# Performance work log

Hardware: AMD Instinct MI355X
Metric: run time of the kernel (lower is better)

## Reference

```python
import jax, jax.numpy as jnp
import numpy as np

N_NODES = 50000
N_EDGES = 800000
IN_DIM = 128
OUT_DIM = 64
NUM_HEADS = 4


def setup_inputs() -> dict:
    key = jax.random.key(0)
    k1, k2, k3, k4 = jax.random.split(key, 4)
    h = jax.random.normal(k1, (N_NODES, IN_DIM), dtype=jnp.float32)
    # Xavier-uniform-like init for each head's weight
    limit = float(np.sqrt(6.0 / (IN_DIM + OUT_DIM)))
    W = jax.random.uniform(k2, (NUM_HEADS, IN_DIM, OUT_DIM), dtype=jnp.float32, minval=-limit, maxval=limit)
    b = jnp.zeros((OUT_DIM,), dtype=jnp.float32)
    src = jax.random.randint(k3, (N_EDGES,), 0, N_NODES, dtype=jnp.int32)
    dst = jax.random.randint(k4, (N_EDGES,), 0, N_NODES, dtype=jnp.int32)
    return {"h": h, "W": W, "b": b, "src": src, "dst": dst}


def reference(h, W, b, src, dst):
    # Multi-head projection averaged over heads: (1/K) * sum_k h @ W_k  -> [N, out_dim]
    hp = jnp.einsum('nd,kdf->nf', h, W) / W.shape[0]
    # copy_src + sum aggregation: scatter-sum messages h[src] into dst nodes
    msgs = hp[src]  # [E, out_dim]
    agg = jax.ops.segment_sum(msgs, dst, num_segments=h.shape[0])  # [N, out_dim]
    return jax.nn.relu(agg + b)
```

## Files before the change

### kernel.cpp

```cpp
#include <hip/hip_runtime.h>

#define N_NODES 50000
#define N_EDGES 800000
#define IN_DIM 128
#define OUT_DIM 64
#define PAD 64

typedef __attribute__((ext_vector_type(8))) short bf16x8;
typedef __attribute__((ext_vector_type(4))) float f32x4;

__device__ inline unsigned short f2bf(float x) {
    unsigned u = __builtin_bit_cast(unsigned, x);
    unsigned r = (u + 0x7FFFu + ((u >> 16) & 1u)) >> 16;
    return (unsigned short)r;
}

__global__ __launch_bounds__(256) void wavgT_kernel(const float* __restrict__ W,
                                                    unsigned short* __restrict__ wT) {
    __shared__ unsigned short lds[64 * 129];
    const int t = threadIdx.x;
    for (int i = t; i < 8192; i += 256) {
        const int d = i >> 6, f = i & 63;
        float s = W[d * 64 + f] + W[8192 + d * 64 + f] +
                  W[16384 + d * 64 + f] + W[24576 + d * 64 + f];
        lds[f * 129 + d] = f2bf(0.25f * s);
    }
    __syncthreads();
    for (int i = t; i < 8192; i += 256) {
        const int f = i >> 7, d = i & 127;
        wT[i] = lds[f * 129 + d];
    }
}

__global__ __launch_bounds__(256) void gemm_mfma_kernel(const float* __restrict__ h,
                                                        const unsigned short* __restrict__ wT,
                                                        unsigned short* __restrict__ hp) {
    const int wave = (blockIdx.x << 2) + (threadIdx.x >> 6);
    const int n0 = wave << 4;
    if (n0 >= N_NODES) return;
    const int lane = threadIdx.x & 63;
    const int lm = lane & 15;
    const int lg = lane >> 4;

    bf16x8 bfrag[4][4];
#pragma unroll
    for (int nt = 0; nt < 4; ++nt)
#pragma unroll
        for (int ks = 0; ks < 4; ++ks)
            bfrag[nt][ks] = *(const bf16x8*)&wT[(nt * 16 + lm) * 128 + ks * 32 + lg * 8];

    f32x4 acc[4];
#pragma unroll
    for (int nt = 0; nt < 4; ++nt) acc[nt] = (f32x4)0.0f;

    const float* hrow = h + (size_t)(n0 + lm) * IN_DIM;
#pragma unroll
    for (int ks = 0; ks < 4; ++ks) {
        const float4 a0 = *(const float4*)&hrow[ks * 32 + lg * 8];
        const float4 a1 = *(const float4*)&hrow[ks * 32 + lg * 8 + 4];
        bf16x8 af;
        af[0] = (short)f2bf(a0.x); af[1] = (short)f2bf(a0.y);
        af[2] = (short)f2bf(a0.z); af[3] = (short)f2bf(a0.w);
        af[4] = (short)f2bf(a1.x); af[5] = (short)f2bf(a1.y);
        af[6] = (short)f2bf(a1.z); af[7] = (short)f2bf(a1.w);
#pragma unroll
        for (int nt = 0; nt < 4; ++nt)
            acc[nt] = __builtin_amdgcn_mfma_f32_16x16x32_bf16(af, bfrag[nt][ks], acc[nt], 0, 0, 0);
    }

#pragma unroll
    for (int nt = 0; nt < 4; ++nt)
#pragma unroll
        for (int r = 0; r < 4; ++r) {
            const int m = lg * 4 + r;
            hp[(size_t)(n0 + m) * 64 + nt * 16 + lm] = f2bf(acc[nt][r]);
        }
}

__global__ __launch_bounds__(256) void fill_kernel(const int* __restrict__ src,
                                                   const int* __restrict__ dst,
                                                   int* __restrict__ cnt,
                                                   unsigned short* __restrict__ esrc) {
    int e = blockIdx.x * 256 + threadIdx.x;
    if (e < N_EDGES) {
        int d = dst[e];
        int pos = atomicAdd(&cnt[d], 1);
        if (pos < PAD) esrc[(size_t)d * PAD + pos] = (unsigned short)src[e];
    }
}

__global__ __launch_bounds__(256) void gather_kernel(const unsigned short* __restrict__ hp,
                                                     const unsigned short* __restrict__ esrc,
                                                     const int* __restrict__ cnt,
                                                     const float* __restrict__ bias,
                                                     float* __restrict__ out) {
    const int n = blockIdx.x * 8 + (threadIdx.x >> 5);
    const int lane = threadIdx.x & 31;
    if (n >= N_NODES) return;

    const unsigned* hp2 = (const unsigned*)hp;
    int deg = cnt[n];
    deg = deg > PAD ? PAD : deg;

    float a0 = 0.f, a1 = 0.f;
    const size_t ebase = (size_t)n * PAD;

    for (int j0 = 0; j0 < deg; j0 += 32) {
        int m = deg - j0;
        if (m > 32) m = 32;
        int sid = (lane < m) ? (int)esrc[ebase + j0 + lane] : 0;
        int j = 0;
        for (; j + 8 <= m; j += 8) {
            unsigned v[8];
#pragma unroll
            for (int k = 0; k < 8; ++k) {
                int s = __shfl(sid, j + k, 32);
                v[k] = hp2[(size_t)s * 32 + lane];
            }
#pragma unroll
            for (int k = 0; k < 8; ++k) {
                a0 += __builtin_bit_cast(float, v[k] << 16);
                a1 += __builtin_bit_cast(float, v[k] & 0xFFFF0000u);
            }
        }
        for (; j < m; ++j) {
            int s = __shfl(sid, j, 32);
            unsigned v = hp2[(size_t)s * 32 + lane];
            a0 += __builtin_bit_cast(float, v << 16);
            a1 += __builtin_bit_cast(float, v & 0xFFFF0000u);
        }
    }

    float2 bv = ((const float2*)bias)[lane];
    float2 o;
    o.x = fmaxf(a0 + bv.x, 0.f);
    o.y = fmaxf(a1 + bv.y, 0.f);
    ((float2*)out)[(size_t)n * 32 + lane] = o;
}

extern "C" void kernel_launch(void* const* d_in, const int* in_sizes, int n_in,
                              void* d_out, int out_size, void* d_ws, size_t ws_size,
                              hipStream_t stream) {
    const float* h   = (const float*)d_in[0];
    const float* W   = (const float*)d_in[1];
    const float* b   = (const float*)d_in[2];
    const int*   src = (const int*)d_in[3];
    const int*   dst = (const int*)d_in[4];
    float* out = (float*)d_out;

    char* p = (char*)d_ws;
    unsigned short* wT = (unsigned short*)p;          p += 32 * 1024;
    unsigned short* hp = (unsigned short*)p;          p += (size_t)N_NODES * OUT_DIM * 2;
    int* cnt = (int*)p;                               p += (size_t)N_NODES * 4;
    unsigned short* esrc = (unsigned short*)p;

    hipMemsetAsync(cnt, 0, (size_t)N_NODES * 4, stream);

    wavgT_kernel<<<1, 256, 0, stream>>>(W, wT);
    gemm_mfma_kernel<<<(N_NODES / 16 + 3) / 4, 256, 0, stream>>>(h, wT, hp);
    fill_kernel<<<(N_EDGES + 255) / 256, 256, 0, stream>>>(src, dst, cnt, esrc);
    gather_kernel<<<(N_NODES + 7) / 8, 256, 0, stream>>>(hp, esrc, cnt, b, out);
}
```

Before: 163.5 us.

## Fuse weight averaging with partitioned edge fill; widen gather to 16-lane groups

Merges the weight-average/transpose kernel with the edge-bucketing fill into one launch. The W work is split across 32 blocks with no LDS, and the fill is split into 8 destination partitions per edge chunk so that the atomics from one block group land in a narrower node range. The gather now gives each node 16 lanes with 8-byte loads, issues 16 loads at once behind a schedule barrier, and masks the extra slots instead of running a remainder loop. The cost is that every edge is read 8 times during the fill, and out-of-range slots issue wasted loads against uninitialized esrc entries.

```diff
diff --git a/kernel.cpp b/kernel.cpp
--- a/kernel.cpp
+++ b/kernel.cpp
@@ -5,6 +5,10 @@
 #define IN_DIM 128
 #define OUT_DIM 64
 #define PAD 64
+#define NPART 6250
+#define FCHUNK 2048
+#define NCHUNK ((N_EDGES + FCHUNK - 1) / FCHUNK)
+#define WAVG_BLOCKS 32
 
 typedef __attribute__((ext_vector_type(8))) short bf16x8;
 typedef __attribute__((ext_vector_type(4))) float f32x4;
@@ -15,20 +19,31 @@
     return (unsigned short)r;
 }
 
-__global__ __launch_bounds__(256) void wavgT_kernel(const float* __restrict__ W,
-                                                    unsigned short* __restrict__ wT) {
-    __shared__ unsigned short lds[64 * 129];
-    const int t = threadIdx.x;
-    for (int i = t; i < 8192; i += 256) {
-        const int d = i >> 6, f = i & 63;
+__global__ __launch_bounds__(256) void wf_kernel(const float* __restrict__ W,
+                                                 unsigned short* __restrict__ wT,
+                                                 const int* __restrict__ src,
+                                                 const int* __restrict__ dst,
+                                                 int* __restrict__ cnt,
+                                                 unsigned short* __restrict__ esrc) {
+    if (blockIdx.x < WAVG_BLOCKS) {
+        const int i = blockIdx.x * 256 + threadIdx.x;
+        const int f = i >> 7, d = i & 127;
         float s = W[d * 64 + f] + W[8192 + d * 64 + f] +
                   W[16384 + d * 64 + f] + W[24576 + d * 64 + f];
-        lds[f * 129 + d] = f2bf(0.25f * s);
+        wT[i] = f2bf(0.25f * s);
+        return;
     }
-    __syncthreads();
-    for (int i = t; i < 8192; i += 256) {
-        const int f = i >> 7, d = i & 127;
-        wT[i] = lds[f * 129 + d];
+    const int bb = blockIdx.x - WAVG_BLOCKS;
+    const int p = bb & 7;
+    const int chunk = bb >> 3;
+    const int e0 = chunk * FCHUNK;
+    for (int e = e0 + threadIdx.x; e < e0 + FCHUNK && e < N_EDGES; e += 256) {
+        const int d = dst[e];
+        const int s = src[e];
+        if (d / NPART == p) {
+            int pos = atomicAdd(&cnt[d], 1);
+            if (pos < PAD) esrc[(size_t)d * PAD + pos] = (unsigned short)s;
+        }
     }
 }
 
@@ -77,65 +92,52 @@
         }
 }
 
-__global__ __launch_bounds__(256) void fill_kernel(const int* __restrict__ src,
-                                                   const int* __restrict__ dst,
-                                                   int* __restrict__ cnt,
-                                                   unsigned short* __restrict__ esrc) {
-    int e = blockIdx.x * 256 + threadIdx.x;
-    if (e < N_EDGES) {
-        int d = dst[e];
-        int pos = atomicAdd(&cnt[d], 1);
-        if (pos < PAD) esrc[(size_t)d * PAD + pos] = (unsigned short)src[e];
-    }
-}
-
 __global__ __launch_bounds__(256) void gather_kernel(const unsigned short* __restrict__ hp,
                                                      const unsigned short* __restrict__ esrc,
                                                      const int* __restrict__ cnt,
                                                      const float* __restrict__ bias,
                                                      float* __restrict__ out) {
-    const int n = blockIdx.x * 8 + (threadIdx.x >> 5);
-    const int lane = threadIdx.x & 31;
+    const int n = blockIdx.x * 16 + (threadIdx.x >> 4);
+    const int l = threadIdx.x & 15;
     if (n >= N_NODES) return;
 
-    const unsigned* hp2 = (const unsigned*)hp;
     int deg = cnt[n];
     deg = deg > PAD ? PAD : deg;
 
-    float a0 = 0.f, a1 = 0.f;
-    const size_t ebase = (size_t)n * PAD;
+    const uint2 sv = ((const uint2*)(esrc + (size_t)n * PAD))[l];
+    const uint2* hp2 = (const uint2*)hp;
 
-    for (int j0 = 0; j0 < deg; j0 += 32) {
-        int m = deg - j0;
-        if (m > 32) m = 32;
-        int sid = (lane < m) ? (int)esrc[ebase + j0 + lane] : 0;
-        int j = 0;
-        for (; j + 8 <= m; j += 8) {
-            unsigned v[8];
+    float a0 = 0.f, a1 = 0.f, a2 = 0.f, a3 = 0.f;
+
+    for (int j0 = 0; j0 < deg; j0 += 16) {
+        const int m = deg - j0;
+        const int b = j0 >> 2;
+        uint2 v[16];
 #pragma unroll
-            for (int k = 0; k < 8; ++k) {
-                int s = __shfl(sid, j + k, 32);
-                v[k] = hp2[(size_t)s * 32 + lane];
+        for (int k = 0; k < 16; ++k) {
+            unsigned w = __shfl(((k >> 1) & 1) ? sv.y : sv.x, b + (k >> 2), 16);
+            unsigned sid = (k & 1) ? (w >> 16) : (w & 0xFFFFu);
+            v[k] = hp2[(size_t)sid * 16 + l];
+        }
+        __builtin_amdgcn_sched_barrier(0);
+#pragma unroll
+        for (int k = 0; k < 16; ++k) {
+            if (k < m) {
+                a0 += __builtin_bit_cast(float, v[k].x << 16);
+                a1 += __builtin_bit_cast(float, v[k].x & 0xFFFF0000u);
+                a2 += __builtin_bit_cast(float, v[k].y << 16);
+                a3 += __builtin_bit_cast(float, v[k].y & 0xFFFF0000u);
             }
-#pragma unroll
-            for (int k = 0; k < 8; ++k) {
-                a0 += __builtin_bit_cast(float, v[k] << 16);
-                a1 += __builtin_bit_cast(float, v[k] & 0xFFFF0000u);
-            }
-        }
-        for (; j < m; ++j) {
-            int s = __shfl(sid, j, 32);
-            unsigned v = hp2[(size_t)s * 32 + lane];
-            a0 += __builtin_bit_cast(float, v << 16);
-            a1 += __builtin_bit_cast(float, v & 0xFFFF0000u);
         }
     }
 
-    float2 bv = ((const float2*)bias)[lane];
-    float2 o;
+    const float4 bv = ((const float4*)bias)[l];
+    float4 o;
     o.x = fmaxf(a0 + bv.x, 0.f);
     o.y = fmaxf(a1 + bv.y, 0.f);
-    ((float2*)out)[(size_t)n * 32 + lane] = o;
+    o.z = fmaxf(a2 + bv.z, 0.f);
+    o.w = fmaxf(a3 + bv.w, 0.f);
+    ((float4*)out)[(size_t)n * 16 + l] = o;
 }
 
 extern "C" void kernel_launch(void* const* d_in, const int* in_sizes, int n_in,
@@ -156,8 +158,7 @@
 
     hipMemsetAsync(cnt, 0, (size_t)N_NODES * 4, stream);
 
-    wavgT_kernel<<<1, 256, 0, stream>>>(W, wT);
+    wf_kernel<<<WAVG_BLOCKS + NCHUNK * 8, 256, 0, stream>>>(W, wT, src, dst, cnt, esrc);
     gemm_mfma_kernel<<<(N_NODES / 16 + 3) / 4, 256, 0, stream>>>(h, wT, hp);
-    fill_kernel<<<(N_EDGES + 255) / 256, 256, 0, stream>>>(src, dst, cnt, esrc);
-    gather_kernel<<<(N_NODES + 7) / 8, 256, 0, stream>>>(hp, esrc, cnt, b, out);
+    gather_kernel<<<(N_NODES + 15) / 16, 256, 0, stream>>>(hp, esrc, cnt, b, out);
 }
```

Result: faster. 145.6 us (-11.0%).

## Bin edges by destination block in LDS and fuse weight prep, GEMM and binning

Applied to the files above, without the earlier changes.

The separate weight-average, GEMM and fill kernels and the counter memset become one launch. The first 49 blocks bucket edges into per-(64-node bin, chunk) lists using LDS histograms and LDS atomics, and the remaining blocks each rebuild the averaged bf16 weight in LDS before running the MFMA projection. A new gather kernel gives one block to each 64-node bin. It reads the bucketed edges, gathers bf16 projected rows, and accumulates them with LDS float atomics before applying bias and ReLU. This removes global per-node atomics, the memset and extra launches. In exchange every GEMM block now redoes the weight reduction, and the gather relies on LDS atomic contention and a per-bucket capacity of 64.

```diff
diff --git a/kernel.cpp b/kernel.cpp
--- a/kernel.cpp
+++ b/kernel.cpp
@@ -4,7 +4,11 @@
 #define N_EDGES 800000
 #define IN_DIM 128
 #define OUT_DIM 64
-#define PAD 64
+#define NBINS 782
+#define FCHUNK 16384
+#define NCHUNK 49
+#define CCAP 64
+#define GEMM_BLOCKS 782
 
 typedef __attribute__((ext_vector_type(8))) short bf16x8;
 typedef __attribute__((ext_vector_type(4))) float f32x4;
@@ -15,30 +19,65 @@
     return (unsigned short)r;
 }
 
-__global__ __launch_bounds__(256) void wavgT_kernel(const float* __restrict__ W,
-                                                    unsigned short* __restrict__ wT) {
-    __shared__ unsigned short lds[64 * 129];
+__global__ __launch_bounds__(256) void fused_kernel(
+    const float* __restrict__ h, const float* __restrict__ W,
+    const int* __restrict__ src, const int* __restrict__ dst,
+    unsigned short* __restrict__ hp, int* __restrict__ cnt2,
+    unsigned* __restrict__ scratch)
+{
+    __shared__ __align__(16) unsigned char smem[16 * 1024];
     const int t = threadIdx.x;
-    for (int i = t; i < 8192; i += 256) {
-        const int d = i >> 6, f = i & 63;
-        float s = W[d * 64 + f] + W[8192 + d * 64 + f] +
-                  W[16384 + d * 64 + f] + W[24576 + d * 64 + f];
-        lds[f * 129 + d] = f2bf(0.25f * s);
+
+    if (blockIdx.x < NCHUNK) {
+        int* hist = (int*)smem;
+        int* cur  = hist + NBINS;
+        for (int i = t; i < NBINS; i += 256) { hist[i] = 0; cur[i] = 0; }
+        __syncthreads();
+        const int blk = blockIdx.x;
+        const int e0 = blk * FCHUNK;
+        const int e1 = (e0 + FCHUNK < N_EDGES) ? e0 + FCHUNK : N_EDGES;
+        for (int e = e0 + t; e < e1; e += 256)
+            atomicAdd(&hist[dst[e] >> 6], 1);
+        __syncthreads();
+        for (int i = t; i < NBINS; i += 256) {
+            int c = hist[i];
+            cnt2[i * NCHUNK + blk] = (c > CCAP) ? CCAP : c;
+        }
+        for (int e = e0 + t; e < e1; e += 256) {
+            const int d = dst[e];
+            const int bin = d >> 6;
+            const int pos = atomicAdd(&cur[bin], 1);
+            if (pos < CCAP)
+                scratch[((size_t)bin * NCHUNK + blk) * CCAP + pos] =
+                    ((unsigned)(d & 63) << 16) | (unsigned)src[e];
+        }
+        return;
+    }
+
+    unsigned short* wT = (unsigned short*)smem;
+    {
+        const float4* W4 = (const float4*)W;
+#pragma unroll
+        for (int r = 0; r < 8; ++r) {
+            const int i4 = t + 256 * r;
+            float4 a = W4[i4], b = W4[i4 + 2048], c = W4[i4 + 4096], d4 = W4[i4 + 6144];
+            float s[4] = {0.25f * (a.x + b.x + c.x + d4.x),
+                          0.25f * (a.y + b.y + c.y + d4.y),
+                          0.25f * (a.z + b.z + c.z + d4.z),
+                          0.25f * (a.w + b.w + c.w + d4.w)};
+#pragma unroll
+            for (int e = 0; e < 4; ++e) {
+                const int i = i4 * 4 + e;
+                wT[(i & 63) * 128 + (i >> 6)] = f2bf(s[e]);
+            }
+        }
     }
     __syncthreads();
-    for (int i = t; i < 8192; i += 256) {
-        const int f = i >> 7, d = i & 127;
-        wT[i] = lds[f * 129 + d];
-    }
-}
 
-__global__ __launch_bounds__(256) void gemm_mfma_kernel(const float* __restrict__ h,
-                                                        const unsigned short* __restrict__ wT,
-                                                        unsigned short* __restrict__ hp) {
-    const int wave = (blockIdx.x << 2) + (threadIdx.x >> 6);
+    const int wave = ((blockIdx.x - NCHUNK) << 2) + (t >> 6);
     const int n0 = wave << 4;
     if (n0 >= N_NODES) return;
-    const int lane = threadIdx.x & 63;
+    const int lane = t & 63;
     const int lm = lane & 15;
     const int lg = lane >> 4;
 
@@ -77,65 +116,63 @@
         }
 }
 
-__global__ __launch_bounds__(256) void fill_kernel(const int* __restrict__ src,
-                                                   const int* __restrict__ dst,
-                                                   int* __restrict__ cnt,
-                                                   unsigned short* __restrict__ esrc) {
-    int e = blockIdx.x * 256 + threadIdx.x;
-    if (e < N_EDGES) {
-        int d = dst[e];
-        int pos = atomicAdd(&cnt[d], 1);
-        if (pos < PAD) esrc[(size_t)d * PAD + pos] = (unsigned short)src[e];
-    }
-}
+__global__ __launch_bounds__(256) void bingather_kernel(
+    const unsigned short* __restrict__ hp, const unsigned* __restrict__ scratch,
+    const int* __restrict__ cnt2, const float* __restrict__ bias,
+    float* __restrict__ out)
+{
+    __shared__ float acc[64 * 64];
+    __shared__ int cnts[NCHUNK];
+    const int t = threadIdx.x;
+    const int b = blockIdx.x;
 
-__global__ __launch_bounds__(256) void gather_kernel(const unsigned short* __restrict__ hp,
-                                                     const unsigned short* __restrict__ esrc,
-                                                     const int* __restrict__ cnt,
-                                                     const float* __restrict__ bias,
-                                                     float* __restrict__ out) {
-    const int n = blockIdx.x * 8 + (threadIdx.x >> 5);
-    const int lane = threadIdx.x & 31;
-    if (n >= N_NODES) return;
+    for (int i = t; i < 4096; i += 256) acc[i] = 0.f;
+    if (t < NCHUNK) cnts[t] = cnt2[b * NCHUNK + t];
+    __syncthreads();
 
-    const unsigned* hp2 = (const unsigned*)hp;
-    int deg = cnt[n];
-    deg = deg > PAD ? PAD : deg;
+    const int lane = t & 63;
+    const int wid = t >> 6;
 
-    float a0 = 0.f, a1 = 0.f;
-    const size_t ebase = (size_t)n * PAD;
-
-    for (int j0 = 0; j0 < deg; j0 += 32) {
-        int m = deg - j0;
-        if (m > 32) m = 32;
-        int sid = (lane < m) ? (int)esrc[ebase + j0 + lane] : 0;
-        int j = 0;
-        for (; j + 8 <= m; j += 8) {
-            unsigned v[8];
+    for (int c = wid; c < NCHUNK; c += 4) {
+        const int mcnt = cnts[c];
+        if (mcnt == 0) continue;
+        const unsigned* sp = scratch + ((size_t)b * NCHUNK + c) * CCAP;
+        const unsigned pk = sp[lane];
+        for (int j0 = 0; j0 < mcnt; j0 += 8) {
+            const int mb = mcnt - j0;
+            unsigned short v[8]; int dl[8];
 #pragma unroll
             for (int k = 0; k < 8; ++k) {
-                int s = __shfl(sid, j + k, 32);
-                v[k] = hp2[(size_t)s * 32 + lane];
+                const unsigned w = __shfl(pk, j0 + k, 64);
+                dl[k] = (int)(w >> 16) & 63;
+                v[k] = hp[(size_t)(w & 0xFFFFu) * 64 + lane];
             }
+            __builtin_amdgcn_sched_barrier(0);
 #pragma unroll
-            for (int k = 0; k < 8; ++k) {
-                a0 += __builtin_bit_cast(float, v[k] << 16);
-                a1 += __builtin_bit_cast(float, v[k] & 0xFFFF0000u);
-            }
-        }
-        for (; j < m; ++j) {
-            int s = __shfl(sid, j, 32);
-            unsigned v = hp2[(size_t)s * 32 + lane];
-            a0 += __builtin_bit_cast(float, v << 16);
-            a1 += __builtin_bit_cast(float, v & 0xFFFF0000u);
+            for (int k = 0; k < 8; ++k)
+                if (k < mb)
+                    atomicAdd(&acc[dl[k] * 64 + lane],
+                              __builtin_bit_cast(float, (unsigned)v[k] << 16));
         }
     }
+    __syncthreads();
 
-    float2 bv = ((const float2*)bias)[lane];
-    float2 o;
-    o.x = fmaxf(a0 + bv.x, 0.f);
-    o.y = fmaxf(a1 + bv.y, 0.f);
-    ((float2*)out)[(size_t)n * 32 + lane] = o;
+    const int n0 = b << 6;
+    int nvalid = N_NODES - n0;
+    if (nvalid > 64) nvalid = 64;
+    const float4* acc4 = (const float4*)acc;
+    const float4* b4 = (const float4*)bias;
+    float4* out4 = (float4*)out;
+    for (int i = t; i < nvalid * 16; i += 256) {
+        float4 a = acc4[i];
+        float4 bb = b4[i & 15];
+        float4 o;
+        o.x = fmaxf(a.x + bb.x, 0.f);
+        o.y = fmaxf(a.y + bb.y, 0.f);
+        o.z = fmaxf(a.z + bb.z, 0.f);
+        o.w = fmaxf(a.w + bb.w, 0.f);
+        out4[(size_t)n0 * 16 + i] = o;
+    }
 }
 
 extern "C" void kernel_launch(void* const* d_in, const int* in_sizes, int n_in,
@@ -149,15 +186,10 @@
     float* out = (float*)d_out;
 
     char* p = (char*)d_ws;
-    unsigned short* wT = (unsigned short*)p;          p += 32 * 1024;
-    unsigned short* hp = (unsigned short*)p;          p += (size_t)N_NODES * OUT_DIM * 2;
-    int* cnt = (int*)p;                               p += (size_t)N_NODES * 4;
-    unsigned short* esrc = (unsigned short*)p;
+    unsigned short* hp = (unsigned short*)p;    p += (size_t)N_NODES * OUT_DIM * 2;
+    int* cnt2 = (int*)p;                        p += (size_t)NBINS * NCHUNK * 4;
+    unsigned* scratch = (unsigned*)p;
 
-    hipMemsetAsync(cnt, 0, (size_t)N_NODES * 4, stream);
-
-    wavgT_kernel<<<1, 256, 0, stream>>>(W, wT);
-    gemm_mfma_kernel<<<(N_NODES / 16 + 3) / 4, 256, 0, stream>>>(h, wT, hp);
-    fill_kernel<<<(N_EDGES + 255) / 256, 256, 0, stream>>>(src, dst, cnt, esrc);
-    gather_kernel<<<(N_NODES + 7) / 8, 256, 0, stream>>>(hp, esrc, cnt, b, out);
+    fused_kernel<<<NCHUNK + GEMM_BLOCKS, 256, 0, stream>>>(h, W, src, dst, hp, cnt2, scratch);
+    bingather_kernel<<<NBINS, 256, 0, stream>>>(hp, scratch, cnt2, b, out);
 }
```

New measurement: 491.4 us. +200.5%, slower.
